# Optimization experiments

Measured on AMD Instinct MI355X. Metric: run time of the kernel, lower is better.

## Reference

```python
import jax, jax.numpy as jnp
import numpy as np
import math

B, A, T = 64, 23, 128          # batch, num_agents, max seq len
D, AE, S, H = 256, 32, 6, 8    # d_model, agent_encoding_dim, static_dim, heads
DK = D // H                     # 32
DM = D + AE                     # 288, MHA q/k/v dim
NEG = -1e10                     # masked_fill constant from source


def sinusoidal_pe(pos, d):
    # pos: int array [...], returns [..., d] standard transformer PE at positions pos
    half = jnp.arange(d // 2, dtype=jnp.float32)
    div = jnp.exp(-half * (math.log(10000.0) * 2.0 / d))          # [d/2]
    ang = pos[..., None].astype(jnp.float32) * div                # [..., d/2]
    return jnp.stack([jnp.sin(ang), jnp.cos(ang)], axis=-1).reshape(*pos.shape, d)


def setup_inputs() -> dict:
    key = jax.random.key(0)
    ks = jax.random.split(key, 20)
    std = 0.02
    data = jax.random.normal(ks[0], (B, A, T), jnp.float32)
    lengths = jax.random.randint(ks[1], (B, A), 0, T + 1).astype(jnp.int32)   # mask arg = lengths
    t = jnp.arange(T, dtype=jnp.int32)
    time = jnp.where(t[None, None, :] < lengths[:, :, None], t[None, None, :], -1)  # [B,A,T], -1 = pad
    static = jax.random.normal(ks[2], (B, S), jnp.float32)
    # per-agent Linear(1, D): weight [A, D], bias [A, D]
    W_embed = std * jax.random.normal(ks[3], (A, D), jnp.float32)
    b_embed = std * jax.random.normal(ks[4], (A, D), jnp.float32)
    E_var = std * jax.random.normal(ks[5], (A, AE), jnp.float32)            # VariateEncoding table
    W_static = std * jax.random.normal(ks[6], (S, D), jnp.float32)
    b_static = jnp.zeros((D,), jnp.float32)
    Wq = std * jax.random.normal(ks[7], (DM, D), jnp.float32); bq = jnp.zeros((D,), jnp.float32)
    Wk = std * jax.random.normal(ks[8], (DM, D), jnp.float32); bk = jnp.zeros((D,), jnp.float32)
    Wv = std * jax.random.normal(ks[9], (DM, D), jnp.float32); bv = jnp.zeros((D,), jnp.float32)
    Wo = std * jax.random.normal(ks[10], (D, DM), jnp.float32); bo = jnp.zeros((DM,), jnp.float32)
    Wg = std * jax.random.normal(ks[11], (DM + D, 1), jnp.float32); bg = jnp.zeros((1,), jnp.float32)
    return dict(data=data, time=time, mask=lengths, static=static,
                W_embed=W_embed, b_embed=b_embed, E_var=E_var,
                W_static=W_static, b_static=b_static,
                Wq=Wq, bq=bq, Wk=Wk, bk=bk, Wv=Wv, bv=bv, Wo=Wo, bo=bo,
                Wg=Wg, bg=bg)


def reference(data, time, mask, static, W_embed, b_embed, E_var, W_static, b_static,
              Wq, bq, Wk, bk, Wv, bv, Wo, bo, Wg, bg):
    lengths = mask                                            # [B,A] sequence lengths
    t = jnp.arange(T)
    valid = t[None, None, :] < lengths[:, :, None]            # [B,A,T] bool
    # mask_matrix[i,:len,:len]=1 double loop -> vectorized outer product
    mask4 = valid[:, :, :, None] & valid[:, :, None, :]       # [B,A,T,T]

    # per-agent Linear(1, D) loop -> batched rank-1 affine, then ReLU
    data_embeds = jax.nn.relu(data[..., None] * W_embed[None, :, None, :]
                              + b_embed[None, :, None, :])    # [B,A,T,D]

    # src_pe: sinusoidal positional encoding at (clamped) time values
    pe = sinusoidal_pe(jnp.maximum(time, 0), D)               # [B,A,T,D]
    src = data_embeds + pe

    # variate (agent-id) embedding concat -> [B,A,T,D+AE]; encoder = identity
    var = jnp.broadcast_to(E_var[None, :, None, :], (B, A, T, AE))
    memory = jnp.concatenate([src, var], axis=-1)             # [B,A,T,DM]

    # time-masked mean pool over T
    time_mask = time >= 0                                     # [B,A,T]
    memory = jnp.where(time_mask[..., None], memory, 0.0)
    counts = time_mask.sum(axis=2).astype(memory.dtype)       # [B,A]
    agentwise = memory.sum(axis=2) / (counts[..., None] + 1e-9)  # [B,A,DM]

    # custom MHA (dim='Time'): q_len = 1 per agent, keys/values over T
    q = jnp.einsum('bae,ed->bad', agentwise, Wq) + bq          # [B,A,D]
    k = jnp.einsum('bate,ed->batd', memory, Wk) + bk           # [B,A,T,D]
    v = jnp.einsum('bate,ed->batd', memory, Wv) + bv
    qh = q.reshape(B, A, H, DK)                                # [B,A,H,DK] (q_len=1 squeezed)
    kh = k.reshape(B, A, T, H, DK).transpose(0, 1, 3, 2, 4)    # [B,A,H,T,DK]
    vh = v.reshape(B, A, T, H, DK).transpose(0, 1, 3, 2, 4)
    scores = jnp.einsum('bahd,bahtd->baht', qh, kh) / math.sqrt(DK)  # [B,A,H,T]
    amask = mask4[:, :, 0, :]                                  # [B,A,T] row 0 of per-agent mask
    scores = jnp.where(amask[:, :, None, :], scores, NEG)
    p = jax.nn.softmax(scores, axis=-1)                        # dropout = eval (identity)
    ctx = jnp.einsum('baht,bahtd->bahd', p, vh).reshape(B, A, D)
    agent_feat = jnp.einsum('bad,de->bae', ctx, Wo) + bo       # [B,A,DM]

    # agent-masked mean pool over agents
    agent_mask = counts > 0                                    # [B,A]
    agent_feat = jnp.where(agent_mask[..., None], agent_feat, 0.0)
    denom = agent_mask.sum(axis=1).astype(agent_feat.dtype) + 1e-9
    aggre = agent_feat.sum(axis=1) / denom[:, None]            # [B,DM]

    static_feat = static @ W_static + b_static                 # [B,D]
    all_feature = jnp.concatenate([aggre, static_feat], axis=-1)  # [B,DM+D]
    return all_feature @ Wg + bg                               # [B,1]


if __name__ == '__main__':
    out = reference(**setup_inputs())
    print(out.shape, jnp.asarray(out).dtype)
```

## Files before the change

kernel.cpp:

```cpp
#include <hip/hip_runtime.h>
#include <math.h>

#define NB 64
#define NA 23
#define NT 128
#define ND 256
#define NAE 32
#define NS 6
#define NH 8
#define NDM 288

#define OFF_PEK    0
#define OFF_PECUM  32768
#define OFF_WKT    65536
#define OFF_VWO    131072
#define OFF_PEMV   133120
#define OFF_EVA    134144
#define OFF_CST    134328
#define OFF_SB     134336

__global__ __launch_bounds__(256) void setup1_kernel(
    const float* __restrict__ Wk, const float* __restrict__ Wv,
    const float* __restrict__ Wo, const float* __restrict__ Wg,
    const float* __restrict__ bv, const float* __restrict__ bo,
    const float* __restrict__ W_static, const float* __restrict__ b_static,
    const float* __restrict__ bg, const float* __restrict__ E_var,
    float* __restrict__ ws)
{
    const int blk = blockIdx.x;
    const int tid = threadIdx.x;
    float* PEcum = ws + OFF_PECUM;
    float* WkT   = ws + OFF_WKT;
    float* VWo   = ws + OFF_VWO;
    float* cst   = ws + OFF_CST;

    if (blk < 128) {
        const int g = tid >> 7, t = tid & 127;
        const int e = blk * 2 + g;
        const int i = e >> 1;
        const float kdiv = 0.07195578415606394f;
        const float dv = expf(-(float)i * kdiv);
        const float ang = (float)t * dv;
        const float v = (e & 1) ? cosf(ang) : sinf(ang);
        __shared__ float buf[256];
        buf[tid] = v;
        #pragma unroll
        for (int s = 1; s < 128; s <<= 1) {
            __syncthreads();
            float add = (t >= s) ? buf[tid - s] : 0.f;
            __syncthreads();
            buf[tid] += add;
        }
        __syncthreads();
        PEcum[t * ND + e] = buf[tid];
    } else if (blk < 384) {
        const int j = blk - 128;
        const float scale = 0.17677669529663687f;
        WkT[j * 256 + tid] = Wk[tid * ND + j] * scale;
    } else if (blk < 392) {
        const int h = blk - 384;
        __shared__ float wog[32];
        __shared__ float vext[32];
        __shared__ float vbS;
        {
            const int jj = tid >> 3, sub = tid & 7;
            const int j = h * 32 + jj;
            float acc = 0.f;
            const int m0 = sub * 36;
            #pragma unroll 4
            for (int m = m0; m < m0 + 36; ++m)
                acc = fmaf(Wo[j * NDM + m], Wg[m], acc);
            acc += __shfl_down(acc, 4, 8);
            acc += __shfl_down(acc, 2, 8);
            acc += __shfl_down(acc, 1, 8);
            if (sub == 0) wog[jj] = acc;
        }
        __syncthreads();
        {
            float acc = 0.f;
            #pragma unroll 8
            for (int jj = 0; jj < 32; ++jj)
                acc = fmaf(Wv[tid * ND + h * 32 + jj], wog[jj], acc);
            VWo[h * 256 + tid] = acc;
        }
        if (tid < 32) {
            float acc = 0.f;
            #pragma unroll 8
            for (int jj = 0; jj < 32; ++jj)
                acc = fmaf(Wv[(256 + tid) * ND + h * 32 + jj], wog[jj], acc);
            vext[tid] = acc;
        }
        if (tid == 0) {
            float acc = 0.f;
            #pragma unroll 8
            for (int jj = 0; jj < 32; ++jj)
                acc = fmaf(bv[h * 32 + jj], wog[jj], acc);
            vbS = acc;
        }
        __syncthreads();
        if (tid < NA) {
            float acc = vbS;
            #pragma unroll 8
            for (int ee = 0; ee < 32; ++ee)
                acc = fmaf(E_var[tid * NAE + ee], vext[ee], acc);
            ws[OFF_EVA + tid * NH + h] = acc;
        }
    } else {
        const int i = tid >> 5, sub = tid & 31;
        float acc = 0.f;
        if (i < 6) {
            for (int m = sub; m < 256; m += 32)
                acc = fmaf(W_static[i * ND + m], Wg[NDM + m], acc);
        } else if (i == 6) {
            for (int m = sub; m < 256; m += 32)
                acc = fmaf(b_static[m], Wg[NDM + m], acc);
        } else {
            for (int m = sub; m < NDM; m += 32)
                acc = fmaf(bo[m], Wg[m], acc);
        }
        #pragma unroll
        for (int off = 16; off > 0; off >>= 1)
            acc += __shfl_down(acc, off, 32);
        if (sub == 0) cst[i] = (i == 6) ? acc + bg[0] : acc;
    }
}

__global__ __launch_bounds__(256) void setup2_kernel(
    const float* __restrict__ Wk, float* __restrict__ ws)
{
    const int t = blockIdx.x;
    const int tid = threadIdx.x;
    __shared__ float peS[256];
    {
        const int i = tid >> 1;
        const float kdiv = 0.07195578415606394f;
        const float dv = expf(-(float)i * kdiv);
        const float ang = (float)t * dv;
        peS[tid] = (tid & 1) ? cosf(ang) : sinf(ang);
    }
    __syncthreads();
    {
        float a0 = 0.f, a1 = 0.f, a2 = 0.f, a3 = 0.f;
        #pragma unroll 4
        for (int e = 0; e < 256; e += 4) {
            a0 = fmaf(peS[e],     Wk[ e      * ND + tid], a0);
            a1 = fmaf(peS[e + 1], Wk[(e + 1) * ND + tid], a1);
            a2 = fmaf(peS[e + 2], Wk[(e + 2) * ND + tid], a2);
            a3 = fmaf(peS[e + 3], Wk[(e + 3) * ND + tid], a3);
        }
        const float scale = 0.17677669529663687f;
        ws[OFF_PEK + t * 256 + tid] = ((a0 + a1) + (a2 + a3)) * scale;
    }
    {
        const int h = tid >> 5, ee = tid & 31;
        const float* vw = ws + OFF_VWO + h * 256;
        float v = 0.f;
        #pragma unroll
        for (int k = 0; k < 8; ++k)
            v = fmaf(peS[ee + 32 * k], vw[ee + 32 * k], v);
        v += __shfl_down(v, 16, 32);
        v += __shfl_down(v, 8, 32);
        v += __shfl_down(v, 4, 32);
        v += __shfl_down(v, 2, 32);
        v += __shfl_down(v, 1, 32);
        if (ee == 0) ws[OFF_PEMV + h * NT + t] = v;
    }
    if (t == 0 && tid < NB) ws[OFF_SB + tid] = 0.f;
}

__global__ __launch_bounds__(256) void main_kernel(
    const float* __restrict__ data, const int* __restrict__ lengths,
    const float* __restrict__ W_embed, const float* __restrict__ b_embed,
    const float* __restrict__ E_var,
    const float* __restrict__ Wq, const float* __restrict__ bq,
    float* __restrict__ ws)
{
    const int wg = blockIdx.x;
    const int a = wg % NA;
    const int b = wg / NA;
    const int tid = threadIdx.x;
    const int L = lengths[wg];

    if (L == 0) return;

    __shared__ float xs[NT];
    __shared__ float agentwise[NDM];
    __shared__ __align__(16) float qs[ND];
    __shared__ float2 Wb[ND];
    __shared__ __align__(16) float combo[ND * 16];
    __shared__ __align__(16) float qkx[NH * NT];
    __shared__ float red[4];

    const float* PEcum = ws + OFF_PECUM;
    const float* WkT   = ws + OFF_WKT;
    const float* VWo   = ws + OFF_VWO;
    const float* cstp  = ws + OFF_CST;

    if (tid < NT) xs[tid] = data[wg * NT + tid];
    __syncthreads();
    {
        const int e = tid;
        const float We = W_embed[a * ND + e];
        const float be = b_embed[a * ND + e];
        Wb[e] = make_float2(We, be);
        float s0 = 0.f, s1 = 0.f, s2 = 0.f, s3 = 0.f;
        int t = 0;
        for (; t + 4 <= L; t += 4) {
            s0 += fmaxf(fmaf(xs[t],     We, be), 0.f);
            s1 += fmaxf(fmaf(xs[t + 1], We, be), 0.f);
            s2 += fmaxf(fmaf(xs[t + 2], We, be), 0.f);
            s3 += fmaxf(fmaf(xs[t + 3], We, be), 0.f);
        }
        for (; t < L; ++t)
            s0 += fmaxf(fmaf(xs[t], We, be), 0.f);
        agentwise[e] = (((s0 + s1) + (s2 + s3)) + PEcum[(L - 1) * ND + e]) / (float)L;
    }
    if (tid < NAE) agentwise[ND + tid] = E_var[a * NAE + tid];
    __syncthreads();

    {
        const int lane = tid & 63;
        const int fc = tid >> 6;
        const float4* Wq4 = (const float4*)Wq;
        float a0 = 0.f, a1 = 0.f, a2 = 0.f, a3 = 0.f;
        const int f0 = fc * 72;
        #pragma unroll 4
        for (int f = f0; f < f0 + 72; ++f) {
            const float ag = agentwise[f];
            const float4 w = Wq4[f * 64 + lane];
            a0 = fmaf(ag, w.x, a0);
            a1 = fmaf(ag, w.y, a1);
            a2 = fmaf(ag, w.z, a2);
            a3 = fmaf(ag, w.w, a3);
        }
        ((float4*)qkx)[fc * 64 + lane] = make_float4(a0, a1, a2, a3);
    }
    __syncthreads();
    qs[tid] = bq[tid] + qkx[tid] + qkx[256 + tid] + qkx[512 + tid] + qkx[768 + tid];
    __syncthreads();

    {
        const int e = tid;
        const float* wcol = WkT + e;
        const int r = e & 3;
        float4* row = (float4*)combo + e * 4;
        float qk[8];
        #pragma unroll
        for (int h = 0; h < 8; ++h) {
            const float* wr = wcol + (h * 32) * 256;
            const float* qh = qs + h * 32;
            float c0 = 0.f, c1 = 0.f;
            #pragma unroll
            for (int j = 0; j < 32; j += 2) {
                c0 = fmaf(wr[ j      * 256], qh[j],     c0);
                c1 = fmaf(wr[(j + 1) * 256], qh[j + 1], c1);
            }
            qk[h] = c0 + c1;
        }
        row[0 ^ r] = make_float4(qk[0], qk[1], qk[2], qk[3]);
        row[1 ^ r] = make_float4(qk[4], qk[5], qk[6], qk[7]);
        row[2 ^ r] = make_float4(VWo[0 * 256 + e], VWo[1 * 256 + e],
                                 VWo[2 * 256 + e], VWo[3 * 256 + e]);
        row[3 ^ r] = make_float4(VWo[4 * 256 + e], VWo[5 * 256 + e],
                                 VWo[6 * 256 + e], VWo[7 * 256 + e]);
    }
    __syncthreads();
    {
        const int h = tid >> 5, t0 = tid & 31;
        const float4* qs4  = (const float4*)qs;
        const float4* PEK4 = (const float4*)(ws + OFF_PEK);
        #pragma unroll
        for (int tt = 0; tt < 4; ++tt) {
            const int t = t0 + tt * 32;
            const float4* pk = PEK4 + t * 64 + h * 8;
            float b0 = 0.f, b1 = 0.f, b2 = 0.f, b3 = 0.f;
            #pragma unroll
            for (int jq = 0; jq < 8; ++jq) {
                const float4 q = qs4[h * 8 + jq];
                const float4 p = pk[jq];
                b0 = fmaf(q.x, p.x, b0);
                b1 = fmaf(q.y, p.y, b1);
                b2 = fmaf(q.z, p.z, b2);
                b3 = fmaf(q.w, p.w, b3);
            }
            qkx[h * NT + t] = (b0 + b1) + (b2 + b3);
        }
    }
    __syncthreads();

    {
        const int t  = tid & 63;
        const int hh = (tid >> 6) & 1;
        const int c  = tid >> 7;
        const int ebase = c * 128;
        const float xt1 = xs[t];
        const float xt2 = xs[t + 64];
        const float4* comboV = (const float4*)combo;
        float aS1[4], aS2[4], aM1[4], aM2[4];
        #pragma unroll
        for (int k = 0; k < 4; ++k) { aS1[k] = 0.f; aS2[k] = 0.f; aM1[k] = 0.f; aM2[k] = 0.f; }

        if (L > 64) {
            #pragma unroll 4
            for (int ee = 0; ee < 128; ++ee) {
                const int e = ebase + ee;
                const int r = e & 3;
                const float2 wb = Wb[e];
                const float m1 = fmaxf(fmaf(xt1, wb.x, wb.y), 0.f);
                const float m2 = fmaxf(fmaf(xt2, wb.x, wb.y), 0.f);
                const float4 cq = comboV[e * 4 + (hh ^ r)];
                const float4 cm = comboV[e * 4 + ((2 | hh) ^ r)];
                aS1[0] = fmaf(m1, cq.x, aS1[0]); aS1[1] = fmaf(m1, cq.y, aS1[1]);
                aS1[2] = fmaf(m1, cq.z, aS1[2]); aS1[3] = fmaf(m1, cq.w, aS1[3]);
                aS2[0] = fmaf(m2, cq.x, aS2[0]); aS2[1] = fmaf(m2, cq.y, aS2[1]);
                aS2[2] = fmaf(m2, cq.z, aS2[2]); aS2[3] = fmaf(m2, cq.w, aS2[3]);
                aM1[0] = fmaf(m1, cm.x, aM1[0]); aM1[1] = fmaf(m1, cm.y, aM1[1]);
                aM1[2] = fmaf(m1, cm.z, aM1[2]); aM1[3] = fmaf(m1, cm.w, aM1[3]);
                aM2[0] = fmaf(m2, cm.x, aM2[0]); aM2[1] = fmaf(m2, cm.y, aM2[1]);
                aM2[2] = fmaf(m2, cm.z, aM2[2]); aM2[3] = fmaf(m2, cm.w, aM2[3]);
            }
        } else {
            #pragma unroll 4
            for (int ee = 0; ee < 128; ++ee) {
                const int e = ebase + ee;
                const int r = e & 3;
                const float2 wb = Wb[e];
                const float m1 = fmaxf(fmaf(xt1, wb.x, wb.y), 0.f);
                const float4 cq = comboV[e * 4 + (hh ^ r)];
                const float4 cm = comboV[e * 4 + ((2 | hh) ^ r)];
                aS1[0] = fmaf(m1, cq.x, aS1[0]); aS1[1] = fmaf(m1, cq.y, aS1[1]);
                aS1[2] = fmaf(m1, cq.z, aS1[2]); aS1[3] = fmaf(m1, cq.w, aS1[3]);
                aM1[0] = fmaf(m1, cm.x, aM1[0]); aM1[1] = fmaf(m1, cm.y, aM1[1]);
                aM1[2] = fmaf(m1, cm.z, aM1[2]); aM1[3] = fmaf(m1, cm.w, aM1[3]);
            }
        }
        __syncthreads();
        float* scF = combo;
        float* mvF = combo + 1024;
        float* pS  = combo + 2048;
        float* pM  = combo + 3072;
        if (c == 1) {
            #pragma unroll
            for (int k = 0; k < 4; ++k) {
                const int h = hh * 4 + k;
                pS[h * NT + t]      = aS1[k];
                pS[h * NT + t + 64] = aS2[k];
                pM[h * NT + t]      = aM1[k];
                pM[h * NT + t + 64] = aM2[k];
            }
        }
        __syncthreads();
        if (c == 0) {
            #pragma unroll
            for (int k = 0; k < 4; ++k) {
                const int h = hh * 4 + k;
                scF[h * NT + t]      = aS1[k] + pS[h * NT + t];
                scF[h * NT + t + 64] = aS2[k] + pS[h * NT + t + 64];
                mvF[h * NT + t]      = aM1[k] + pM[h * NT + t];
                mvF[h * NT + t + 64] = aM2[k] + pM[h * NT + t + 64];
            }
        }
    }
    __syncthreads();

    {
        const float* sc   = combo;
        const float* mvb  = combo + 1024;
        const float* pemv = ws + OFF_PEMV;
        const int wv = tid >> 6, lane = tid & 63;
        float wsum = 0.f;
        for (int hh = 0; hh < 2; ++hh) {
            const int h = wv * 2 + hh;
            float s1 = (lane < L) ? sc[h * NT + lane] + qkx[h * NT + lane] : -3e38f;
            float s2 = (lane + 64 < L) ? sc[h * NT + 64 + lane] + qkx[h * NT + 64 + lane] : -3e38f;
            float mx = fmaxf(s1, s2);
            #pragma unroll
            for (int off = 32; off > 0; off >>= 1)
                mx = fmaxf(mx, __shfl_down(mx, off, 64));
            mx = __shfl(mx, 0, 64);
            const float vbv = ws[OFF_EVA + a * NH + h];
            float e1 = (lane < L) ? __expf(s1 - mx) : 0.f;
            float e2 = (lane + 64 < L) ? __expf(s2 - mx) : 0.f;
            float num = e1 * (mvb[h * NT + lane] + pemv[h * NT + lane] + vbv);
            num = fmaf(e2, mvb[h * NT + 64 + lane] + pemv[h * NT + 64 + lane] + vbv, num);
            float den = e1 + e2;
            #pragma unroll
            for (int off = 32; off > 0; off >>= 1) {
                num += __shfl_down(num, off, 64);
                den += __shfl_down(den, off, 64);
            }
            if (lane == 0) wsum += num / den;
        }
        if (lane == 0) red[wv] = wsum;
    }
    __syncthreads();
    if (tid == 0)
        atomicAdd(ws + OFF_SB + b, cstp[7] + red[0] + red[1] + red[2] + red[3]);
}

__global__ __launch_bounds__(64) void final_kernel(
    const float* __restrict__ statics, const int* __restrict__ lengths,
    const float* __restrict__ ws, float* __restrict__ out)
{
    const int b = threadIdx.x;
    const float* cst = ws + OFF_CST;
    int n = 0;
    for (int a = 0; a < NA; ++a)
        if (lengths[b * NA + a] > 0) ++n;
    float o = ws[OFF_SB + b] / ((float)n + 1e-9f);
    #pragma unroll
    for (int i = 0; i < NS; ++i)
        o = fmaf(statics[b * NS + i], cst[i], o);
    o += cst[6];
    out[b] = o;
}

extern "C" void kernel_launch(void* const* d_in, const int* in_sizes, int n_in,
                              void* d_out, int out_size, void* d_ws, size_t ws_size,
                              hipStream_t stream) {
    const float* data     = (const float*)d_in[0];
    const int*   mask     = (const int*)d_in[2];
    const float* statics  = (const float*)d_in[3];
    const float* W_embed  = (const float*)d_in[4];
    const float* b_embed  = (const float*)d_in[5];
    const float* E_var    = (const float*)d_in[6];
    const float* W_static = (const float*)d_in[7];
    const float* b_static = (const float*)d_in[8];
    const float* Wq       = (const float*)d_in[9];
    const float* bq       = (const float*)d_in[10];
    const float* Wk       = (const float*)d_in[11];
    const float* Wv       = (const float*)d_in[13];
    const float* bv       = (const float*)d_in[14];
    const float* Wo       = (const float*)d_in[15];
    const float* bo       = (const float*)d_in[16];
    const float* Wg       = (const float*)d_in[17];
    const float* bg       = (const float*)d_in[18];
    float* out = (float*)d_out;
    float* ws  = (float*)d_ws;

    setup1_kernel<<<dim3(393), dim3(256), 0, stream>>>(Wk, Wv, Wo, Wg, bv, bo,
                                                       W_static, b_static, bg, E_var, ws);
    setup2_kernel<<<dim3(128), dim3(256), 0, stream>>>(Wk, ws);
    main_kernel<<<dim3(NB * NA), dim3(256), 0, stream>>>(data, mask, W_embed, b_embed,
                                                         E_var, Wq, bq, ws);
    final_kernel<<<dim3(1), dim3(64), 0, stream>>>(statics, mask, ws, out);
}
```

Measured before the change: 174.2 us.

## Process two agent workgroups per 512-thread block to share weight loads

Each block now handles two (batch, agent) pairs with 512 threads. The Wq projection, WkT·q products, VWo loads and PE·q products are computed for both halves at once, so each weight value read from global memory is used for two agents. This roughly halves the weight traffic per agent. In exchange it doubles shared memory per block, which may lower occupancy. Agents with zero length can no longer exit early and must take part in the shared barriers.

```diff
diff --git a/kernel.cpp b/kernel.cpp
--- a/kernel.cpp
+++ b/kernel.cpp
@@ -168,144 +168,166 @@
     if (t == 0 && tid < NB) ws[OFF_SB + tid] = 0.f;
 }
 
-__global__ __launch_bounds__(256) void main_kernel(
+__global__ __launch_bounds__(512) void main_kernel(
     const float* __restrict__ data, const int* __restrict__ lengths,
     const float* __restrict__ W_embed, const float* __restrict__ b_embed,
     const float* __restrict__ E_var,
     const float* __restrict__ Wq, const float* __restrict__ bq,
     float* __restrict__ ws)
 {
-    const int wg = blockIdx.x;
-    const int a = wg % NA;
-    const int b = wg / NA;
-    const int tid = threadIdx.x;
-    const int L = lengths[wg];
-
-    if (L == 0) return;
-
-    __shared__ float xs[NT];
-    __shared__ float agentwise[NDM];
-    __shared__ __align__(16) float qs[ND];
-    __shared__ float2 Wb[ND];
-    __shared__ __align__(16) float combo[ND * 16];
-    __shared__ __align__(16) float qkx[NH * NT];
-    __shared__ float red[4];
+    const int pair = blockIdx.x;
+    const int tid  = threadIdx.x;
+    const int half = tid >> 8;
+    const int lt   = tid & 255;
+    const int wgh  = pair * 2 + half;
+    const int ah   = wgh % NA;
+    const int bh   = wgh / NA;
+    const int Lh   = lengths[wgh];
+
+    __shared__ float xs[2][NT];
+    __shared__ float ag[2][NDM];
+    __shared__ __align__(16) float qs[2][ND];
+    __shared__ float2 Wb[2][ND];
+    __shared__ __align__(16) float combo[2][ND * 16];
+    __shared__ __align__(16) float qkx[2][NH * NT];
+    __shared__ float red[2][4];
 
     const float* PEcum = ws + OFF_PECUM;
     const float* WkT   = ws + OFF_WKT;
     const float* VWo   = ws + OFF_VWO;
     const float* cstp  = ws + OFF_CST;
 
-    if (tid < NT) xs[tid] = data[wg * NT + tid];
-    __syncthreads();
-    {
-        const int e = tid;
-        const float We = W_embed[a * ND + e];
-        const float be = b_embed[a * ND + e];
-        Wb[e] = make_float2(We, be);
-        float s0 = 0.f, s1 = 0.f, s2 = 0.f, s3 = 0.f;
-        int t = 0;
-        for (; t + 4 <= L; t += 4) {
-            s0 += fmaxf(fmaf(xs[t],     We, be), 0.f);
-            s1 += fmaxf(fmaf(xs[t + 1], We, be), 0.f);
-            s2 += fmaxf(fmaf(xs[t + 2], We, be), 0.f);
-            s3 += fmaxf(fmaf(xs[t + 3], We, be), 0.f);
-        }
-        for (; t < L; ++t)
-            s0 += fmaxf(fmaf(xs[t], We, be), 0.f);
-        agentwise[e] = (((s0 + s1) + (s2 + s3)) + PEcum[(L - 1) * ND + e]) / (float)L;
-    }
-    if (tid < NAE) agentwise[ND + tid] = E_var[a * NAE + tid];
-    __syncthreads();
-
-    {
-        const int lane = tid & 63;
-        const int fc = tid >> 6;
-        const float4* Wq4 = (const float4*)Wq;
+    if (lt < NT) xs[half][lt] = data[wgh * NT + lt];
+    __syncthreads();
+    {
+        const int e = lt;
+        if (Lh > 0) {
+            const float We = W_embed[ah * ND + e];
+            const float be = b_embed[ah * ND + e];
+            Wb[half][e] = make_float2(We, be);
+            float s0 = 0.f, s1 = 0.f, s2 = 0.f, s3 = 0.f;
+            int t = 0;
+            for (; t + 4 <= Lh; t += 4) {
+                s0 += fmaxf(fmaf(xs[half][t],     We, be), 0.f);
+                s1 += fmaxf(fmaf(xs[half][t + 1], We, be), 0.f);
+                s2 += fmaxf(fmaf(xs[half][t + 2], We, be), 0.f);
+                s3 += fmaxf(fmaf(xs[half][t + 3], We, be), 0.f);
+            }
+            for (; t < Lh; ++t)
+                s0 += fmaxf(fmaf(xs[half][t], We, be), 0.f);
+            ag[half][e] = (((s0 + s1) + (s2 + s3)) + PEcum[(Lh - 1) * ND + e]) / (float)Lh;
+        } else {
+            Wb[half][e] = make_float2(0.f, 0.f);
+            ag[half][e] = 0.f;
+        }
+    }
+    if (lt < NAE) ag[half][ND + lt] = (Lh > 0) ? E_var[ah * NAE + lt] : 0.f;
+    __syncthreads();
+
+    {
+        const int j = lt;
+        const int f0 = half * 144;
         float a0 = 0.f, a1 = 0.f, a2 = 0.f, a3 = 0.f;
-        const int f0 = fc * 72;
         #pragma unroll 4
-        for (int f = f0; f < f0 + 72; ++f) {
-            const float ag = agentwise[f];
-            const float4 w = Wq4[f * 64 + lane];
-            a0 = fmaf(ag, w.x, a0);
-            a1 = fmaf(ag, w.y, a1);
-            a2 = fmaf(ag, w.z, a2);
-            a3 = fmaf(ag, w.w, a3);
-        }
-        ((float4*)qkx)[fc * 64 + lane] = make_float4(a0, a1, a2, a3);
-    }
-    __syncthreads();
-    qs[tid] = bq[tid] + qkx[tid] + qkx[256 + tid] + qkx[512 + tid] + qkx[768 + tid];
-    __syncthreads();
-
-    {
-        const int e = tid;
-        const float* wcol = WkT + e;
+        for (int f = f0; f < f0 + 144; f += 2) {
+            const float w0 = Wq[f * ND + j];
+            const float w1 = Wq[(f + 1) * ND + j];
+            a0 = fmaf(ag[0][f],     w0, a0);
+            a2 = fmaf(ag[0][f + 1], w1, a2);
+            a1 = fmaf(ag[1][f],     w0, a1);
+            a3 = fmaf(ag[1][f + 1], w1, a3);
+        }
+        float* Csc = &combo[0][0];
+        Csc[half * 512 +       j] = a0 + a2;
+        Csc[half * 512 + 256 + j] = a1 + a3;
+    }
+    __syncthreads();
+    {
+        const float* Csc = &combo[0][0];
+        qs[half][lt] = bq[lt] + Csc[half * 256 + lt] + Csc[512 + half * 256 + lt];
+    }
+    __syncthreads();
+
+    {
+        const int e = lt;
+        const int hb = half;
+        const float* wr = WkT + (hb * 128) * 256 + e;
+        float qk0[4], qk1[4];
+        #pragma unroll
+        for (int h4 = 0; h4 < 4; ++h4) {
+            const float* q0 = qs[0] + hb * 128 + h4 * 32;
+            const float* q1 = qs[1] + hb * 128 + h4 * 32;
+            float c00 = 0.f, c01 = 0.f, c10 = 0.f, c11 = 0.f;
+            #pragma unroll
+            for (int jj = 0; jj < 32; jj += 2) {
+                const float wa = wr[(h4 * 32 + jj)     * 256];
+                const float wb = wr[(h4 * 32 + jj + 1) * 256];
+                c00 = fmaf(wa, q0[jj],     c00);
+                c01 = fmaf(wb, q0[jj + 1], c01);
+                c10 = fmaf(wa, q1[jj],     c10);
+                c11 = fmaf(wb, q1[jj + 1], c11);
+            }
+            qk0[h4] = c00 + c01;
+            qk1[h4] = c10 + c11;
+        }
         const int r = e & 3;
-        float4* row = (float4*)combo + e * 4;
-        float qk[8];
-        #pragma unroll
-        for (int h = 0; h < 8; ++h) {
-            const float* wr = wcol + (h * 32) * 256;
-            const float* qh = qs + h * 32;
-            float c0 = 0.f, c1 = 0.f;
-            #pragma unroll
-            for (int j = 0; j < 32; j += 2) {
-                c0 = fmaf(wr[ j      * 256], qh[j],     c0);
-                c1 = fmaf(wr[(j + 1) * 256], qh[j + 1], c1);
-            }
-            qk[h] = c0 + c1;
-        }
-        row[0 ^ r] = make_float4(qk[0], qk[1], qk[2], qk[3]);
-        row[1 ^ r] = make_float4(qk[4], qk[5], qk[6], qk[7]);
-        row[2 ^ r] = make_float4(VWo[0 * 256 + e], VWo[1 * 256 + e],
-                                 VWo[2 * 256 + e], VWo[3 * 256 + e]);
-        row[3 ^ r] = make_float4(VWo[4 * 256 + e], VWo[5 * 256 + e],
-                                 VWo[6 * 256 + e], VWo[7 * 256 + e]);
-    }
-    __syncthreads();
-    {
-        const int h = tid >> 5, t0 = tid & 31;
-        const float4* qs4  = (const float4*)qs;
+        float4* row0 = (float4*)(&combo[0][0]) + e * 4;
+        float4* row1 = (float4*)(&combo[1][0]) + e * 4;
+        row0[hb ^ r] = make_float4(qk0[0], qk0[1], qk0[2], qk0[3]);
+        row1[hb ^ r] = make_float4(qk1[0], qk1[1], qk1[2], qk1[3]);
+        const float4 vw = make_float4(VWo[(hb * 4 + 0) * 256 + e],
+                                      VWo[(hb * 4 + 1) * 256 + e],
+                                      VWo[(hb * 4 + 2) * 256 + e],
+                                      VWo[(hb * 4 + 3) * 256 + e]);
+        row0[(2 | hb) ^ r] = vw;
+        row1[(2 | hb) ^ r] = vw;
+    }
+    {
+        const int h = tid >> 6;
+        const int tq = tid & 63;
+        const float4* qs40 = (const float4*)qs[0] + h * 8;
+        const float4* qs41 = (const float4*)qs[1] + h * 8;
         const float4* PEK4 = (const float4*)(ws + OFF_PEK);
         #pragma unroll
-        for (int tt = 0; tt < 4; ++tt) {
-            const int t = t0 + tt * 32;
+        for (int tt = 0; tt < 2; ++tt) {
+            const int t = tq + tt * 64;
             const float4* pk = PEK4 + t * 64 + h * 8;
-            float b0 = 0.f, b1 = 0.f, b2 = 0.f, b3 = 0.f;
+            float b00 = 0.f, b01 = 0.f, b02 = 0.f, b03 = 0.f;
+            float b10 = 0.f, b11 = 0.f, b12 = 0.f, b13 = 0.f;
             #pragma unroll
             for (int jq = 0; jq < 8; ++jq) {
-                const float4 q = qs4[h * 8 + jq];
                 const float4 p = pk[jq];
-                b0 = fmaf(q.x, p.x, b0);
-                b1 = fmaf(q.y, p.y, b1);
-                b2 = fmaf(q.z, p.z, b2);
-                b3 = fmaf(q.w, p.w, b3);
-            }
-            qkx[h * NT + t] = (b0 + b1) + (b2 + b3);
-        }
-    }
-    __syncthreads();
-
-    {
-        const int t  = tid & 63;
-        const int hh = (tid >> 6) & 1;
-        const int c  = tid >> 7;
+                const float4 q0 = qs40[jq];
+                const float4 q1 = qs41[jq];
+                b00 = fmaf(q0.x, p.x, b00); b01 = fmaf(q0.y, p.y, b01);
+                b02 = fmaf(q0.z, p.z, b02); b03 = fmaf(q0.w, p.w, b03);
+                b10 = fmaf(q1.x, p.x, b10); b11 = fmaf(q1.y, p.y, b11);
+                b12 = fmaf(q1.z, p.z, b12); b13 = fmaf(q1.w, p.w, b13);
+            }
+            qkx[0][h * NT + t] = (b00 + b01) + (b02 + b03);
+            qkx[1][h * NT + t] = (b10 + b11) + (b12 + b13);
+        }
+    }
+    __syncthreads();
+
+    {
+        const int t  = lt & 63;
+        const int hh = (lt >> 6) & 1;
+        const int c  = lt >> 7;
         const int ebase = c * 128;
-        const float xt1 = xs[t];
-        const float xt2 = xs[t + 64];
-        const float4* comboV = (const float4*)combo;
+        const float xt1 = xs[half][t];
+        const float xt2 = xs[half][t + 64];
+        const float4* comboV = (const float4*)(&combo[half][0]);
         float aS1[4], aS2[4], aM1[4], aM2[4];
         #pragma unroll
         for (int k = 0; k < 4; ++k) { aS1[k] = 0.f; aS2[k] = 0.f; aM1[k] = 0.f; aM2[k] = 0.f; }
 
-        if (L > 64) {
+        if (Lh > 64) {
             #pragma unroll 4
             for (int ee = 0; ee < 128; ++ee) {
                 const int e = ebase + ee;
                 const int r = e & 3;
-                const float2 wb = Wb[e];
+                const float2 wb = Wb[half][e];
                 const float m1 = fmaxf(fmaf(xt1, wb.x, wb.y), 0.f);
                 const float m2 = fmaxf(fmaf(xt2, wb.x, wb.y), 0.f);
                 const float4 cq = comboV[e * 4 + (hh ^ r)];
@@ -319,12 +341,12 @@
                 aM2[0] = fmaf(m2, cm.x, aM2[0]); aM2[1] = fmaf(m2, cm.y, aM2[1]);
                 aM2[2] = fmaf(m2, cm.z, aM2[2]); aM2[3] = fmaf(m2, cm.w, aM2[3]);
             }
-        } else {
+        } else if (Lh > 0) {
             #pragma unroll 4
             for (int ee = 0; ee < 128; ++ee) {
                 const int e = ebase + ee;
                 const int r = e & 3;
-                const float2 wb = Wb[e];
+                const float2 wb = Wb[half][e];
                 const float m1 = fmaxf(fmaf(xt1, wb.x, wb.y), 0.f);
                 const float4 cq = comboV[e * 4 + (hh ^ r)];
                 const float4 cm = comboV[e * 4 + ((2 | hh) ^ r)];
@@ -335,10 +357,10 @@
             }
         }
         __syncthreads();
-        float* scF = combo;
-        float* mvF = combo + 1024;
-        float* pS  = combo + 2048;
-        float* pM  = combo + 3072;
+        float* scF = &combo[half][0];
+        float* mvF = scF + 1024;
+        float* pS  = scF + 2048;
+        float* pM  = scF + 3072;
         if (c == 1) {
             #pragma unroll
             for (int k = 0; k < 4; ++k) {
@@ -363,24 +385,24 @@
     }
     __syncthreads();
 
-    {
-        const float* sc   = combo;
-        const float* mvb  = combo + 1024;
+    if (Lh > 0) {
+        const float* sc   = &combo[half][0];
+        const float* mvb  = sc + 1024;
         const float* pemv = ws + OFF_PEMV;
-        const int wv = tid >> 6, lane = tid & 63;
+        const int wv = lt >> 6, lane = lt & 63;
         float wsum = 0.f;
-        for (int hh = 0; hh < 2; ++hh) {
-            const int h = wv * 2 + hh;
-            float s1 = (lane < L) ? sc[h * NT + lane] + qkx[h * NT + lane] : -3e38f;
-            float s2 = (lane + 64 < L) ? sc[h * NT + 64 + lane] + qkx[h * NT + 64 + lane] : -3e38f;
+        for (int hh2 = 0; hh2 < 2; ++hh2) {
+            const int h = wv * 2 + hh2;
+            float s1 = (lane < Lh) ? sc[h * NT + lane] + qkx[half][h * NT + lane] : -3e38f;
+            float s2 = (lane + 64 < Lh) ? sc[h * NT + 64 + lane] + qkx[half][h * NT + 64 + lane] : -3e38f;
             float mx = fmaxf(s1, s2);
             #pragma unroll
             for (int off = 32; off > 0; off >>= 1)
                 mx = fmaxf(mx, __shfl_down(mx, off, 64));
             mx = __shfl(mx, 0, 64);
-            const float vbv = ws[OFF_EVA + a * NH + h];
-            float e1 = (lane < L) ? __expf(s1 - mx) : 0.f;
-            float e2 = (lane + 64 < L) ? __expf(s2 - mx) : 0.f;
+            const float vbv = ws[OFF_EVA + ah * NH + h];
+            float e1 = (lane < Lh) ? __expf(s1 - mx) : 0.f;
+            float e2 = (lane + 64 < Lh) ? __expf(s2 - mx) : 0.f;
             float num = e1 * (mvb[h * NT + lane] + pemv[h * NT + lane] + vbv);
             num = fmaf(e2, mvb[h * NT + 64 + lane] + pemv[h * NT + 64 + lane] + vbv, num);
             float den = e1 + e2;
@@ -391,11 +413,12 @@
             }
             if (lane == 0) wsum += num / den;
         }
-        if (lane == 0) red[wv] = wsum;
-    }
-    __syncthreads();
-    if (tid == 0)
-        atomicAdd(ws + OFF_SB + b, cstp[7] + red[0] + red[1] + red[2] + red[3]);
+        if (lane == 0) red[half][wv] = wsum;
+    }
+    __syncthreads();
+    if (lt == 0 && Lh > 0)
+        atomicAdd(ws + OFF_SB + bh,
+                  cstp[7] + red[half][0] + red[half][1] + red[half][2] + red[half][3]);
 }
 
 __global__ __launch_bounds__(64) void final_kernel(
@@ -441,7 +464,7 @@
     setup1_kernel<<<dim3(393), dim3(256), 0, stream>>>(Wk, Wv, Wo, Wg, bv, bo,
                                                        W_static, b_static, bg, E_var, ws);
     setup2_kernel<<<dim3(128), dim3(256), 0, stream>>>(Wk, ws);
-    main_kernel<<<dim3(NB * NA), dim3(256), 0, stream>>>(data, mask, W_embed, b_embed,
-                                                         E_var, Wq, bq, ws);
+    main_kernel<<<dim3(NB * NA / 2), dim3(512), 0, stream>>>(data, mask, W_embed, b_embed,
+                                                             E_var, Wq, bq, ws);
     final_kernel<<<dim3(1), dim3(64), 0, stream>>>(statics, mask, ws, out);
 }
```

Measured after the change: 173.6 us. Within noise of the previous version (-0.4%).
